# Kernel optimization log

Measured on AMD Instinct MI355X. Metric: run time of the kernel, lower is better.

## Reference

```python
import jax, jax.numpy as jnp
import numpy as np

EMB = 1024
HEADS = 16
DH = EMB // HEADS
EPS = 1e-5


def _layernorm(x, w, b):
    mean = jnp.mean(x, axis=-1, keepdims=True)
    var = jnp.mean((x - mean) ** 2, axis=-1, keepdims=True)  # unbiased=False
    return w * (x - mean) / jnp.sqrt(var + EPS) + b


def _gelu_tanh(x):
    c = jnp.sqrt(jnp.asarray(2.0 / jnp.pi, x.dtype))
    return 0.5 * x * (1.0 + jnp.tanh(c * (x + 0.044715 * x ** 3)))


def setup_inputs() -> dict:
    key = jax.random.key(0)
    ks = jax.random.split(key, 8)
    B, N = 2, 2048
    s = lambda fan_in: 1.0 / np.sqrt(fan_in)
    # weights stored as [in, out] (torch Linear applied as x @ W.T == x @ W_here)
    return {
        "x": jax.random.normal(ks[0], (B, N, EMB), jnp.float32),
        "ln1_w": jnp.ones((EMB,), jnp.float32),
        "ln1_b": jnp.zeros((EMB,), jnp.float32),
        "w_qkv": jax.random.normal(ks[1], (EMB, 3 * EMB), jnp.float32) * s(EMB),  # qkv_bias=False
        "w_attn_proj": jax.random.normal(ks[2], (EMB, EMB), jnp.float32) * s(EMB),
        "b_attn_proj": jnp.zeros((EMB,), jnp.float32),
        "ln2_w": jnp.ones((EMB,), jnp.float32),
        "ln2_b": jnp.zeros((EMB,), jnp.float32),
        "w_fc": jax.random.normal(ks[3], (EMB, 4 * EMB), jnp.float32) * s(EMB),
        "b_fc": jnp.zeros((4 * EMB,), jnp.float32),
        "w_proj": jax.random.normal(ks[4], (4 * EMB, EMB), jnp.float32) * s(4 * EMB),
        "b_proj": jnp.zeros((EMB,), jnp.float32),
    }


def reference(x, ln1_w, ln1_b, w_qkv, w_attn_proj, b_attn_proj,
              ln2_w, ln2_b, w_fc, b_fc, w_proj, b_proj):
    B, N, _ = x.shape
    # --- attention sublayer (pre-LN) ---
    h = _layernorm(x, ln1_w, ln1_b)
    qkv = h @ w_qkv  # [B,N,3E]
    q, k, v = jnp.split(qkv, 3, axis=-1)
    # [B,H,N,Dh]
    q = q.reshape(B, N, HEADS, DH).transpose(0, 2, 1, 3)
    k = k.reshape(B, N, HEADS, DH).transpose(0, 2, 1, 3)
    v = v.reshape(B, N, HEADS, DH).transpose(0, 2, 1, 3)
    scores = jnp.einsum("bhqd,bhkd->bhqk", q, k) * (DH ** -0.5)
    causal = jnp.tril(jnp.ones((N, N), bool))
    scores = jnp.where(causal, scores, -jnp.inf)
    attn = jax.nn.softmax(scores, axis=-1)  # attn_pdrop=0 (eval)
    ctx = jnp.einsum("bhqk,bhkd->bhqd", attn, v)
    ctx = ctx.transpose(0, 2, 1, 3).reshape(B, N, EMB)
    x = x + (ctx @ w_attn_proj + b_attn_proj)  # resid_pdrop=0
    # --- MLP sublayer (pre-LN) ---
    h = _layernorm(x, ln2_w, ln2_b)
    h = _gelu_tanh(h @ w_fc + b_fc)
    x = x + (h @ w_proj + b_proj)
    return x
```

## Files before the change

kernel.cpp:

```cpp
#include <hip/hip_runtime.h>
#include <stdint.h>

#define EMB 1024
#define NHEAD 16
#define DH 64
#define SEQ 2048
#define NTOK 4096

typedef __attribute__((ext_vector_type(8))) short s16x8;
typedef __attribute__((ext_vector_type(4))) short s16x4;
typedef __attribute__((ext_vector_type(4))) float f32x4;
typedef __attribute__((ext_vector_type(4))) unsigned short u16x4;

__device__ __forceinline__ unsigned short f2bf(float f){
    union { float f; unsigned int u; } v; v.f = f;
    unsigned int r = v.u + 0x7fffu + ((v.u >> 16) & 1u);
    return (unsigned short)(r >> 16);
}

__device__ __forceinline__ f32x4 mfma16(s16x8 a, s16x8 b, f32x4 c){
    return __builtin_amdgcn_mfma_f32_16x16x32_bf16(a, b, c, 0, 0, 0);
}

__device__ __forceinline__ void gload16(const void* g, void* l){
    __builtin_amdgcn_global_load_lds((const __attribute__((address_space(1))) void*)g,
                                     (__attribute__((address_space(3))) void*)l, 16, 0, 0);
}

__device__ __forceinline__ s16x8 cat8(s16x4 a, s16x4 b){
    s16x8 r;
    r[0]=a[0]; r[1]=a[1]; r[2]=a[2]; r[3]=a[3];
    r[4]=b[0]; r[5]=b[1]; r[6]=b[2]; r[7]=b[3];
    return r;
}

__global__ __launch_bounds__(256) void convT_kernel(const float* __restrict__ in,
                                                    unsigned short* __restrict__ out,
                                                    int R, int C){
    __shared__ float tile[32][33];
    const int c0 = blockIdx.x * 32, r0 = blockIdx.y * 32;
    const int tx = threadIdx.x, ty = threadIdx.y;
    #pragma unroll
    for (int k = 0; k < 4; ++k)
        tile[ty*4+k][tx] = in[(long)(r0 + ty*4 + k) * C + c0 + tx];
    __syncthreads();
    #pragma unroll
    for (int k = 0; k < 4; ++k)
        out[(long)(c0 + ty*4 + k) * R + r0 + tx] = f2bf(tile[tx][ty*4+k]);
}

__global__ __launch_bounds__(256) void vT_kernel(const unsigned short* __restrict__ qkv,
                                                 unsigned short* __restrict__ vtg){
    __shared__ unsigned short tile[64*64];
    const int bh = blockIdx.y, b = bh >> 4, h = bh & 15;
    const int n0 = blockIdx.x * 64;
    const int t = threadIdx.x;
    const int nr = t >> 3, c0 = (t & 7) * 8;
    #pragma unroll
    for (int hh = 0; hh < 2; ++hh){
        const int n = nr + hh*32;
        uint4 vv = *(const uint4*)&qkv[(long)(b*SEQ + n0 + n)*3072 + 2048 + h*64 + c0];
        *(uint4*)((char*)tile + n*128 + ((c0*2) ^ (((n>>3)&7)<<4))) = vv;
    }
    __syncthreads();
    #pragma unroll
    for (int hh = 0; hh < 2; ++hh){
        const int d = nr + hh*32;
        union { unsigned short u[8]; uint4 v; } tmp;
        #pragma unroll
        for (int j = 0; j < 8; ++j){
            const int n = c0 + j;
            tmp.u[j] = *(const unsigned short*)((char*)tile + n*128 + ((d*2) ^ (((n>>3)&7)<<4)));
        }
        *(uint4*)&vtg[((long)bh*64 + d)*2048 + n0 + c0] = tmp.v;
    }
}

__global__ __launch_bounds__(256) void ln_kernel(const float* __restrict__ x,
                                                 const float* __restrict__ w,
                                                 const float* __restrict__ b,
                                                 unsigned short* __restrict__ out){
    const int row = blockIdx.x, tid = threadIdx.x;
    const float4 v = ((const float4*)(x + (long)row * EMB))[tid];
    float s  = v.x + v.y + v.z + v.w;
    float ss = v.x*v.x + v.y*v.y + v.z*v.z + v.w*v.w;
    #pragma unroll
    for (int off = 32; off >= 1; off >>= 1){
        s  += __shfl_xor(s,  off, 64);
        ss += __shfl_xor(ss, off, 64);
    }
    __shared__ float ps[4], pss[4];
    const int wv = tid >> 6;
    if ((tid & 63) == 0){ ps[wv] = s; pss[wv] = ss; }
    __syncthreads();
    s  = ps[0] + ps[1] + ps[2] + ps[3];
    ss = pss[0] + pss[1] + pss[2] + pss[3];
    const float mean = s * (1.0f/EMB);
    const float var  = ss * (1.0f/EMB) - mean*mean;
    const float rstd = rsqrtf(var + 1e-5f);
    const float4 wv4 = ((const float4*)w)[tid];
    const float4 bv4 = ((const float4*)b)[tid];
    u16x4 o;
    o[0] = f2bf((v.x - mean) * rstd * wv4.x + bv4.x);
    o[1] = f2bf((v.y - mean) * rstd * wv4.y + bv4.y);
    o[2] = f2bf((v.z - mean) * rstd * wv4.z + bv4.z);
    o[3] = f2bf((v.w - mean) * rstd * wv4.w + bv4.w);
    *(u16x4*)(out + (long)row * EMB + tid * 4) = o;
}

template<int EPI, int BM, int BN>
__global__ __launch_bounds__(256) void gemm_kernel(const unsigned short* __restrict__ A,
                                                   const unsigned short* __restrict__ Bt,
                                                   const float* __restrict__ bias,
                                                   const float* __restrict__ resid,
                                                   void* __restrict__ outv,
                                                   int M, int N, int K){
    constexpr int FI = BM / 32;
    constexpr int FJ = BN / 32;
    __shared__ unsigned short As[2][BM * 32];
    __shared__ unsigned short Bs[2][BN * 32];
    const int tid  = threadIdx.x;
    const int lane = tid & 63, w = tid >> 6;
    const int lm = lane & 15, g = lane >> 4;
    const int wr = w >> 1, wc = w & 1;
    const int m0 = blockIdx.y * BM, n0 = blockIdx.x * BN;
    const int r_st = tid >> 2, q_st = (tid & 3) * 8;

    f32x4 zero = {0.0f, 0.0f, 0.0f, 0.0f};
    f32x4 acc[FI][FJ];
    #pragma unroll
    for (int i = 0; i < FI; ++i)
        #pragma unroll
        for (int j = 0; j < FJ; ++j) acc[i][j] = zero;

    auto stage = [&](int kt, int bu){
        #pragma unroll
        for (int p = 0; p < BM/64; ++p)
            gload16(&A[(long)(m0 + r_st + p*64) * K + kt + q_st],
                    (char*)&As[bu][0] + p*4096 + w*1024);
        #pragma unroll
        for (int p = 0; p < BN/64; ++p)
            gload16(&Bt[(long)(n0 + r_st + p*64) * K + kt + q_st],
                    (char*)&Bs[bu][0] + p*4096 + w*1024);
    };

    stage(0, 0);
    int cur = 0;
    const int nkt = K / 32;
    for (int t = 0; t < nkt; ++t){
        __syncthreads();
        if (t + 1 < nkt) stage((t+1)*32, cur ^ 1);
        s16x8 af[FI], bf[FJ];
        #pragma unroll
        for (int i = 0; i < FI; ++i)
            af[i] = *(const s16x8*)&As[cur][(wr*(BM/2) + i*16 + lm)*32 + g*8];
        #pragma unroll
        for (int j = 0; j < FJ; ++j)
            bf[j] = *(const s16x8*)&Bs[cur][(wc*(BN/2) + j*16 + lm)*32 + g*8];
        #pragma unroll
        for (int i = 0; i < FI; ++i)
            #pragma unroll
            for (int j = 0; j < FJ; ++j)
                acc[i][j] = mfma16(af[i], bf[j], acc[i][j]);
        cur ^= 1;
    }

    #pragma unroll
    for (int i = 0; i < FI; ++i){
        #pragma unroll
        for (int r = 0; r < 4; ++r){
            const int row = m0 + wr*(BM/2) + i*16 + 4*g + r;
            #pragma unroll
            for (int j = 0; j < FJ; ++j){
                const int col = n0 + wc*(BN/2) + j*16 + lm;
                const float v = acc[i][j][r];
                if (EPI == 0){
                    ((unsigned short*)outv)[(long)row * N + col] = f2bf(v);
                } else if (EPI == 1){
                    ((float*)outv)[(long)row * N + col] =
                        v + bias[col] + resid[(long)row * N + col];
                } else {
                    const float xx = v + bias[col];
                    const float z = 0.7978845608f * (xx + 0.044715f * xx * xx * xx);
                    const float gg = xx / (1.0f + __expf(-2.0f * z));
                    ((unsigned short*)outv)[(long)row * N + col] = f2bf(gg);
                }
            }
        }
    }
}

__global__ __launch_bounds__(256) void attn_kernel(const unsigned short* __restrict__ qkv,
                                                   const unsigned short* __restrict__ vtg,
                                                   unsigned short* __restrict__ ctx){
    __shared__ unsigned short Ks[2][4096];
    __shared__ unsigned short Vs[2][4096];
    const int pair = blockIdx.x, bh = blockIdx.y;
    const int b = bh >> 4, h = bh & 15;
    const int tid = threadIdx.x, lane = tid & 63, w = tid >> 6;
    const int lm = lane & 15, g = lane >> 4;
    const long qkvb = (long)b * SEQ * 3072;
    const unsigned short* kglob = qkv + qkvb + 1024 + h*64;
    const unsigned short* vglob = vtg + (long)bh * 64 * 2048;

    const int srow = tid >> 3;
    const int soff = (tid & 7) * 16;
    f32x4 zero = {0.0f, 0.0f, 0.0f, 0.0f};

    #pragma unroll 1
    for (int grp = 0; grp < 2; ++grp){
        const int qg = (grp == 0) ? pair : (31 - pair);
        const int q0 = qg * 64;
        const int nt = qg + 1;
        const int qrow = q0 + w*16 + lm;

        const unsigned short* qrp = qkv + qkvb + (long)qrow*3072 + h*64;
        const s16x8 qf0 = *(const s16x8*)(qrp + g*8);
        const s16x8 qf1 = *(const s16x8*)(qrp + 32 + g*8);

        f32x4 o[4];
        #pragma unroll
        for (int d = 0; d < 4; ++d) o[d] = zero;
        float mrun = -3e38f, lrun = 0.0f;

        auto stage = [&](int t, int bu){
            const int kv0 = t * 64;
            #pragma unroll
            for (int hh = 0; hh < 2; ++hh){
                const int row = srow + hh*32;
                const int sw  = soff ^ ((row & 7) << 4);
                gload16(kglob + (long)(kv0 + row)*3072 + (sw >> 1),
                        (char*)&Ks[bu][0] + hh*4096 + w*1024);
                gload16(vglob + (long)row*2048 + kv0 + (sw >> 1),
                        (char*)&Vs[bu][0] + hh*4096 + w*1024);
            }
        };

        __syncthreads();
        stage(0, 0);
        int cur = 0;
        #pragma unroll 1
        for (int t = 0; t < nt; ++t){
            __syncthreads();
            if (t + 1 < nt) stage(t + 1, cur ^ 1);

            const char* Kb = (const char*)&Ks[cur][0];
            const int sw = (lm & 7) << 4;
            f32x4 sc[4];
            #pragma unroll
            for (int s = 0; s < 4; ++s){
                const char* rp = Kb + (s*16 + lm)*128;
                s16x8 kf0 = *(const s16x8*)(rp + ((g*16) ^ sw));
                s16x8 kf1 = *(const s16x8*)(rp + ((64 + g*16) ^ sw));
                f32x4 a = mfma16(kf0, qf0, zero);
                sc[s] = mfma16(kf1, qf1, a);
            }

            const bool diag = (t == nt - 1);
            float p[4][4];
            float mx = -3e38f;
            #pragma unroll
            for (int s = 0; s < 4; ++s)
                #pragma unroll
                for (int r = 0; r < 4; ++r){
                    float vv = sc[s][r] * 0.125f;
                    if (diag && (s*16 + 4*g + r > w*16 + lm)) vv = -3e38f;
                    p[s][r] = vv;
                    mx = fmaxf(mx, vv);
                }
            mx = fmaxf(mx, __shfl_xor(mx, 16, 64));
            mx = fmaxf(mx, __shfl_xor(mx, 32, 64));
            const float mnew = fmaxf(mrun, mx);
            const float corr = __expf(mrun - mnew);
            float rs = 0.0f;
            #pragma unroll
            for (int s = 0; s < 4; ++s)
                #pragma unroll
                for (int r = 0; r < 4; ++r){
                    const float e = __expf(p[s][r] - mnew);
                    p[s][r] = e;
                    rs += e;
                }
            rs += __shfl_xor(rs, 16, 64);
            rs += __shfl_xor(rs, 32, 64);
            lrun = lrun * corr + rs;
            mrun = mnew;
            #pragma unroll
            for (int d = 0; d < 4; ++d) o[d] *= corr;

            s16x8 pf0, pf1;
            #pragma unroll
            for (int e = 0; e < 8; ++e){
                pf0[e] = (short)f2bf(p[(e>>2)][e&3]);
                pf1[e] = (short)f2bf(p[2 + (e>>2)][e&3]);
            }

            const char* Vb = (const char*)&Vs[cur][0];
            #pragma unroll
            for (int d = 0; d < 4; ++d){
                const char* vrp = Vb + (d*16 + lm)*128;
                s16x4 a0 = *(const s16x4*)(vrp + ((g*8) ^ sw));
                s16x4 a1 = *(const s16x4*)(vrp + ((32 + g*8) ^ sw));
                o[d] = mfma16(cat8(a0, a1), pf0, o[d]);
                s16x4 b0 = *(const s16x4*)(vrp + ((64 + g*8) ^ sw));
                s16x4 b1 = *(const s16x4*)(vrp + ((96 + g*8) ^ sw));
                o[d] = mfma16(cat8(b0, b1), pf1, o[d]);
            }
            cur ^= 1;
        }

        const float inv = 1.0f / lrun;
        unsigned short* cw = ctx + (long)(b*SEQ + qrow)*EMB + h*DH + 4*g;
        #pragma unroll
        for (int d = 0; d < 4; ++d){
            u16x4 ov;
            ov[0] = f2bf(o[d][0]*inv); ov[1] = f2bf(o[d][1]*inv);
            ov[2] = f2bf(o[d][2]*inv); ov[3] = f2bf(o[d][3]*inv);
            *(u16x4*)(cw + d*16) = ov;
        }
    }
}

extern "C" void kernel_launch(void* const* d_in, const int* in_sizes, int n_in,
                              void* d_out, int out_size, void* d_ws, size_t ws_size,
                              hipStream_t stream){
    const float* x     = (const float*)d_in[0];
    const float* ln1_w = (const float*)d_in[1];
    const float* ln1_b = (const float*)d_in[2];
    const float* w_qkv = (const float*)d_in[3];
    const float* w_ap  = (const float*)d_in[4];
    const float* b_ap  = (const float*)d_in[5];
    const float* ln2_w = (const float*)d_in[6];
    const float* ln2_b = (const float*)d_in[7];
    const float* w_fc  = (const float*)d_in[8];
    const float* b_fc  = (const float*)d_in[9];
    const float* w_pr  = (const float*)d_in[10];
    const float* b_pr  = (const float*)d_in[11];
    float* out = (float*)d_out;

    char* ws = (char*)d_ws;
    unsigned short* wqkvT = (unsigned short*)(ws + 0);
    unsigned short* wapT  = (unsigned short*)(ws + 6291456);
    unsigned short* wfcT  = (unsigned short*)(ws + 8388608);
    unsigned short* wprT  = (unsigned short*)(ws + 16777216);
    unsigned short* h1    = (unsigned short*)(ws + 25165824);
    unsigned short* vtg   = (unsigned short*)(ws + 25165824);
    unsigned short* qkv   = (unsigned short*)(ws + 33554432);
    unsigned short* ctx   = (unsigned short*)(ws + 58720256);
    float*          x1    = (float*)(ws + 67108864);
    unsigned short* h2    = (unsigned short*)(ws + 83886080);
    unsigned short* afc   = (unsigned short*)(ws + 92274688);

    dim3 b32(32, 8, 1);
    convT_kernel<<<dim3(3072/32, 1024/32), b32, 0, stream>>>(w_qkv, wqkvT, 1024, 3072);
    convT_kernel<<<dim3(1024/32, 1024/32), b32, 0, stream>>>(w_ap,  wapT,  1024, 1024);
    convT_kernel<<<dim3(4096/32, 1024/32), b32, 0, stream>>>(w_fc,  wfcT,  1024, 4096);
    convT_kernel<<<dim3(1024/32, 4096/32), b32, 0, stream>>>(w_pr,  wprT,  4096, 1024);

    ln_kernel<<<NTOK, 256, 0, stream>>>(x, ln1_w, ln1_b, h1);

    gemm_kernel<0,128,128><<<dim3(3072/128, NTOK/128), 256, 0, stream>>>(
        h1, wqkvT, nullptr, nullptr, qkv, NTOK, 3072, 1024);

    vT_kernel<<<dim3(SEQ/64, 32), 256, 0, stream>>>(qkv, vtg);

    attn_kernel<<<dim3(16, 32), 256, 0, stream>>>(qkv, vtg, ctx);

    gemm_kernel<1,128,64><<<dim3(1024/64, NTOK/128), 256, 0, stream>>>(
        ctx, wapT, b_ap, x, x1, NTOK, 1024, 1024);

    ln_kernel<<<NTOK, 256, 0, stream>>>(x1, ln2_w, ln2_b, h2);

    gemm_kernel<2,128,128><<<dim3(4096/128, NTOK/128), 256, 0, stream>>>(
        h2, wfcT, b_fc, nullptr, afc, NTOK, 4096, 1024);

    gemm_kernel<1,128,64><<<dim3(1024/64, NTOK/128), 256, 0, stream>>>(
        afc, wprT, b_pr, x1, out, NTOK, 1024, 4096);
}
```

Measured before the change: 286.0 us.

## Use 64x64 per-wave GEMM tiles and XCD-aware block remapping

Each GEMM wavefront now computes a fixed 64x64 output tile (4x4 MFMAs). The N=1024 GEMMs drop to 2 waves per block, and the staging loads are generalized to the wave count. Block IDs are also remapped so consecutive IDs spread across the 8 XCDs, which should improve L2 reuse of neighbouring tiles. In exchange, the smaller blocks on the projection GEMMs give fewer waves to hide latency, and the remap assumes the block count divides by 8.

Result: no change. 291.5 us (+1.9%).

```diff
diff --git a/kernel.cpp b/kernel.cpp
--- a/kernel.cpp
+++ b/kernel.cpp
@@ -108,40 +108,44 @@
     *(u16x4*)(out + (long)row * EMB + tid * 4) = o;
 }
 
-template<int EPI, int BM, int BN>
-__global__ __launch_bounds__(256) void gemm_kernel(const unsigned short* __restrict__ A,
-                                                   const unsigned short* __restrict__ Bt,
-                                                   const float* __restrict__ bias,
-                                                   const float* __restrict__ resid,
-                                                   void* __restrict__ outv,
-                                                   int M, int N, int K){
-    constexpr int FI = BM / 32;
-    constexpr int FJ = BN / 32;
+template<int EPI, int BM, int BN, int NW>
+__global__ __launch_bounds__(NW*64) void gemm_kernel(const unsigned short* __restrict__ A,
+                                                     const unsigned short* __restrict__ Bt,
+                                                     const float* __restrict__ bias,
+                                                     const float* __restrict__ resid,
+                                                     void* __restrict__ outv,
+                                                     int M, int N, int K){
+    constexpr int WR = BM / 64;
+    constexpr int WC = BN / 64;
     __shared__ unsigned short As[2][BM * 32];
     __shared__ unsigned short Bs[2][BN * 32];
     const int tid  = threadIdx.x;
     const int lane = tid & 63, w = tid >> 6;
     const int lm = lane & 15, g = lane >> 4;
-    const int wr = w >> 1, wc = w & 1;
-    const int m0 = blockIdx.y * BM, n0 = blockIdx.x * BN;
-    const int r_st = tid >> 2, q_st = (tid & 3) * 8;
+    const int wr = w / WC, wc = w % WC;
+
+    const int gx = gridDim.x;
+    const int nwg = gx * gridDim.y;
+    int id = blockIdx.y * gx + blockIdx.x;
+    id = (id & 7) * (nwg >> 3) + (id >> 3);
+    const int m0 = (id / gx) * BM, n0 = (id % gx) * BN;
 
     f32x4 zero = {0.0f, 0.0f, 0.0f, 0.0f};
-    f32x4 acc[FI][FJ];
-    #pragma unroll
-    for (int i = 0; i < FI; ++i)
-        #pragma unroll
-        for (int j = 0; j < FJ; ++j) acc[i][j] = zero;
+    f32x4 acc[4][4];
+    #pragma unroll
+    for (int i = 0; i < 4; ++i)
+        #pragma unroll
+        for (int j = 0; j < 4; ++j) acc[i][j] = zero;
 
     auto stage = [&](int kt, int bu){
         #pragma unroll
-        for (int p = 0; p < BM/64; ++p)
-            gload16(&A[(long)(m0 + r_st + p*64) * K + kt + q_st],
-                    (char*)&As[bu][0] + p*4096 + w*1024);
-        #pragma unroll
-        for (int p = 0; p < BN/64; ++p)
-            gload16(&Bt[(long)(n0 + r_st + p*64) * K + kt + q_st],
-                    (char*)&Bs[bu][0] + p*4096 + w*1024);
+        for (int p = 0; p < BM/(NW*16); ++p)
+            gload16(&A[(long)(m0 + p*NW*16 + (tid>>2)) * K + kt + (tid&3)*8],
+                    (char*)&As[bu][0] + p*(NW*1024) + tid*16);
+        #pragma unroll
+        for (int p = 0; p < BN/(NW*16); ++p)
+            gload16(&Bt[(long)(n0 + p*NW*16 + (tid>>2)) * K + kt + (tid&3)*8],
+                    (char*)&Bs[bu][0] + p*(NW*1024) + tid*16);
     };
 
     stage(0, 0);
@@ -150,29 +154,29 @@
     for (int t = 0; t < nkt; ++t){
         __syncthreads();
         if (t + 1 < nkt) stage((t+1)*32, cur ^ 1);
-        s16x8 af[FI], bf[FJ];
-        #pragma unroll
-        for (int i = 0; i < FI; ++i)
-            af[i] = *(const s16x8*)&As[cur][(wr*(BM/2) + i*16 + lm)*32 + g*8];
-        #pragma unroll
-        for (int j = 0; j < FJ; ++j)
-            bf[j] = *(const s16x8*)&Bs[cur][(wc*(BN/2) + j*16 + lm)*32 + g*8];
-        #pragma unroll
-        for (int i = 0; i < FI; ++i)
-            #pragma unroll
-            for (int j = 0; j < FJ; ++j)
+        s16x8 af[4], bf[4];
+        #pragma unroll
+        for (int i = 0; i < 4; ++i)
+            af[i] = *(const s16x8*)&As[cur][(wr*64 + i*16 + lm)*32 + g*8];
+        #pragma unroll
+        for (int j = 0; j < 4; ++j)
+            bf[j] = *(const s16x8*)&Bs[cur][(wc*64 + j*16 + lm)*32 + g*8];
+        #pragma unroll
+        for (int i = 0; i < 4; ++i)
+            #pragma unroll
+            for (int j = 0; j < 4; ++j)
                 acc[i][j] = mfma16(af[i], bf[j], acc[i][j]);
         cur ^= 1;
     }
 
     #pragma unroll
-    for (int i = 0; i < FI; ++i){
+    for (int i = 0; i < 4; ++i){
         #pragma unroll
         for (int r = 0; r < 4; ++r){
-            const int row = m0 + wr*(BM/2) + i*16 + 4*g + r;
-            #pragma unroll
-            for (int j = 0; j < FJ; ++j){
-                const int col = n0 + wc*(BN/2) + j*16 + lm;
+            const int row = m0 + wr*64 + i*16 + 4*g + r;
+            #pragma unroll
+            for (int j = 0; j < 4; ++j){
+                const int col = n0 + wc*64 + j*16 + lm;
                 const float v = acc[i][j][r];
                 if (EPI == 0){
                     ((unsigned short*)outv)[(long)row * N + col] = f2bf(v);
@@ -359,21 +363,21 @@
 
     ln_kernel<<<NTOK, 256, 0, stream>>>(x, ln1_w, ln1_b, h1);
 
-    gemm_kernel<0,128,128><<<dim3(3072/128, NTOK/128), 256, 0, stream>>>(
+    gemm_kernel<0,128,128,4><<<dim3(3072/128, NTOK/128), 256, 0, stream>>>(
         h1, wqkvT, nullptr, nullptr, qkv, NTOK, 3072, 1024);
 
     vT_kernel<<<dim3(SEQ/64, 32), 256, 0, stream>>>(qkv, vtg);
 
     attn_kernel<<<dim3(16, 32), 256, 0, stream>>>(qkv, vtg, ctx);
 
-    gemm_kernel<1,128,64><<<dim3(1024/64, NTOK/128), 256, 0, stream>>>(
+    gemm_kernel<1,128,64,2><<<dim3(1024/64, NTOK/128), 128, 0, stream>>>(
         ctx, wapT, b_ap, x, x1, NTOK, 1024, 1024);
 
     ln_kernel<<<NTOK, 256, 0, stream>>>(x1, ln2_w, ln2_b, h2);
 
-    gemm_kernel<2,128,128><<<dim3(4096/128, NTOK/128), 256, 0, stream>>>(
+    gemm_kernel<2,128,128,4><<<dim3(4096/128, NTOK/128), 256, 0, stream>>>(
         h2, wfcT, b_fc, nullptr, afc, NTOK, 4096, 1024);
 
-    gemm_kernel<1,128,64><<<dim3(1024/64, NTOK/128), 256, 0, stream>>>(
+    gemm_kernel<1,128,64,2><<<dim3(1024/64, NTOK/128), 128, 0, stream>>>(
         afc, wprT, b_pr, x1, out, NTOK, 1024, 4096);
 }
```
